# Optimization experiments

Hardware: AMD Instinct MI355X
Metric: run time of the kernel (lower is better)

The kernel has to match this reference:

```python
import jax, jax.numpy as jnp
import numpy as np

HIDDEN = 256
OUT_CH = 3
OMEGA_0 = 30.0
PATCH = 5


def setup_inputs() -> dict:
    key = jax.random.key(0)
    ks = jax.random.split(key, 9)
    B, C, H, W = 1, 128, 256, 256
    in_dim = C * PATCH * PATCH + 2  # 3202
    xi = jax.random.normal(ks[0], (B, C, H, W), dtype=jnp.float32)

    def lin(kw, kb, fi, fo):
        s = 1.0 / np.sqrt(fi)
        Wm = jax.random.uniform(kw, (fi, fo), jnp.float32, -s, s)
        bm = jax.random.uniform(kb, (fo,), jnp.float32, -s, s)
        return Wm, bm

    W1, b1 = lin(ks[1], ks[2], in_dim, HIDDEN)
    W2, b2 = lin(ks[3], ks[4], HIDDEN, HIDDEN)
    W3, b3 = lin(ks[5], ks[6], HIDDEN, HIDDEN)
    W4, b4 = lin(ks[7], ks[8], HIDDEN, OUT_CH)
    return {"xi": xi, "W1": W1, "b1": b1, "W2": W2, "b2": b2,
            "W3": W3, "b3": b3, "W4": W4, "b4": b4}


def _make_coords(B, H, W, dtype):
    # normalized pixel coords in [-1, 1], shape [B*H*W, 2]
    ys = jnp.linspace(-1.0, 1.0, H, dtype=dtype)
    xs = jnp.linspace(-1.0, 1.0, W, dtype=dtype)
    gy, gx = jnp.meshgrid(ys, xs, indexing="ij")
    coords = jnp.stack([gy, gx], axis=-1).reshape(H * W, 2)
    return jnp.tile(coords, (B, 1))


def reference(xi, W1, b1, W2, b2, W3, b3, W4, b4):
    B, C, H, W = xi.shape
    # im2col 5x5 patch gather (zero pad), like F.unfold with padding=2
    patches = jax.lax.conv_general_dilated_patches(
        xi, (PATCH, PATCH), (1, 1), "SAME")  # [B, C*25, H, W]
    feat = jnp.transpose(patches, (0, 2, 3, 1)).reshape(B * H * W, C * PATCH * PATCH)
    coords = _make_coords(B, H, W, xi.dtype)
    x = jnp.concatenate([feat, coords], axis=-1)  # [N, 3202]
    h = jnp.sin(OMEGA_0 * (x @ W1 + b1))
    h = jnp.sin(OMEGA_0 * (h @ W2 + b2))
    h = jnp.sin(OMEGA_0 * (h @ W3 + b3))
    out = h @ W4 + b4  # [N, 3]
    rgb = out.reshape(B, H, W, OUT_CH).transpose(0, 3, 1, 2)
    return rgb
```

## Files before the change

kernel.cpp:

```cpp
#include <hip/hip_runtime.h>
#include <math.h>
#include <stdint.h>

typedef _Float16 f16;
typedef _Float16 f16x8 __attribute__((ext_vector_type(8)));
typedef float f32x4 __attribute__((ext_vector_type(4)));
typedef unsigned short u16;
typedef u16 u16x8 __attribute__((ext_vector_type(8)));

#define HID 256
#define NS1C 100
#define NS2 8
#define NPX 65536
#define BPXG 256
#define NBG (NPX/BPXG)
#define SPAD 260
#define NSP (SPAD*SPAD)

#define OFF_W1C 0
#define SZ_W1C  ((size_t)NS1C*32768)
#define OFF_W2  SZ_W1C
#define SZ_W2   ((size_t)NS2*32768)
#define OFF_W3  (OFF_W2+SZ_W2)
#define OFF_XH  ((size_t)4194304)
#define SZ_XP   ((size_t)NSP*128*2)
#define OFF_XL  (OFF_XH + SZ_XP)
#define OFF_HH  (OFF_XL + SZ_XP)
#define SZ_HP   ((size_t)NPX*HID*2)
#define OFF_HL  (OFF_HH + SZ_HP)

__device__ inline void split2(float v, u16& h, u16& l){
  f16 hv = (f16)v;
  f16 lv = (f16)(v - (float)hv);
  h = __builtin_bit_cast(u16, hv);
  l = __builtin_bit_cast(u16, lv);
}

__global__ void prep_w(const float* __restrict__ W, int Kact, int nStages,
                       u16* __restrict__ outp){
  int t = blockIdx.x*256 + threadIdx.x;
  if (t >= nStages*1024) return;
  int s = t >> 10, r = t & 1023;
  int w = r >> 8, nf = (r >> 6) & 3, l = r & 63;
  int col = w*64 + nf*16 + (l & 15);
  int kb  = s*32 + (l >> 4)*8;
  u16x8 hv, lv;
  #pragma unroll
  for (int j = 0; j < 8; ++j){
    int k = kb + j;
    float v = (k < Kact) ? W[(size_t)k*HID + col] : 0.f;
    u16 h, lo; split2(v, h, lo);
    hv[j] = h; lv[j] = lo;
  }
  size_t U0 = ((((size_t)s*4 + w)*4 + nf)*2 + 0)*64 + l;
  *(u16x8*)(outp + U0*8)      = hv;
  *(u16x8*)(outp + (U0+64)*8) = lv;
}

__global__ void prep_w1c(const float* __restrict__ W1, u16* __restrict__ outp){
  int t = blockIdx.x*256 + threadIdx.x;
  if (t >= NS1C*1024) return;
  int s = t >> 10, r = t & 1023;
  int w = r >> 8, nf = (r >> 6) & 3, l = r & 63;
  int col = w*64 + nf*16 + (l & 15);
  int tap = s >> 2, cg = s & 3;
  int cb  = cg*32 + (l >> 4)*8;
  u16x8 hv, lv;
  #pragma unroll
  for (int j = 0; j < 8; ++j){
    int c = cb + j;
    float v = W1[(size_t)(c*25 + tap)*HID + col];
    u16 h, lo; split2(v, h, lo);
    hv[j] = h; lv[j] = lo;
  }
  size_t U0 = ((((size_t)s*4 + w)*4 + nf)*2 + 0)*64 + l;
  *(u16x8*)(outp + U0*8)      = hv;
  *(u16x8*)(outp + (U0+64)*8) = lv;
}

__global__ __launch_bounds__(256)
void prep_x(const float* __restrict__ xi, u16* __restrict__ Xh, u16* __restrict__ Xl){
  int sp = blockIdx.x*256 + threadIdx.x;
  if (sp >= NSP) return;
  int py = sp / SPAD;
  int px = sp - py*SPAD;
  bool inb = (py >= 2) & (py < 258) & (px >= 2) & (px < 258);
  const float* xin = xi + ((size_t)(py-2)<<8) + (px-2);
  #pragma unroll 4
  for (int cg = 0; cg < 16; ++cg){
    u16x8 hv, lv;
    #pragma unroll
    for (int j = 0; j < 8; ++j){
      float v = inb ? xin[((size_t)(cg*8 + j))<<16] : 0.f;
      u16 h, l; split2(v, h, l); hv[j] = h; lv[j] = l;
    }
    *(u16x8*)(Xh + (size_t)sp*128 + cg*8) = hv;
    *(u16x8*)(Xl + (size_t)sp*128 + cg*8) = lv;
  }
}

template<int MODE>
__global__ __launch_bounds__(512, 2)
void gemm(const u16* __restrict__ Ah, const u16* __restrict__ Al,
          const u16* __restrict__ Wp, const float* __restrict__ W1,
          const float* __restrict__ bias, u16* __restrict__ Hh, u16* __restrict__ Hl,
          const float* __restrict__ W4, const float* __restrict__ b4,
          float* __restrict__ out, int nt)
{
  __shared__ __align__(16) u16 Ab[2][16384];
  __shared__ __align__(16) u16 Bb[2][16384];

  const int tid  = threadIdx.x;
  const int lane = tid & 63;
  const int wv   = tid >> 6;
  const int wm   = wv >> 2, wn = wv & 3;

  int bid = blockIdx.x;
  bid = (bid & 7)*(NBG/8) + (bid >> 3);
  const int pxb = bid * BPXG;
  const int y   = bid;

  f32x4 acc[8][4];
  #pragma unroll
  for (int a=0;a<8;a++)
    #pragma unroll
    for (int bq=0;bq<4;bq++) acc[a][bq] = f32x4{0.f,0.f,0.f,0.f};

#define A_STAGE(S, BUF) do { \
    _Pragma("unroll") \
    for (int u=0;u<2;++u){ \
      const int mfb = wv*2 + u; \
      size_t off; \
      if (MODE == 0){ \
        const int tap = (S) >> 2, cg = (S) & 3; \
        const int dy = tap/5, dx = tap - 5*dy; \
        const int sp = (y + dy)*SPAD + dx + mfb*16 + (lane & 15); \
        off = (size_t)sp*128 + cg*32 + (lane >> 4)*8; \
      } else { \
        const int px = pxb + mfb*16 + (lane & 15); \
        off = (size_t)px*HID + (S)*32 + (lane >> 4)*8; \
      } \
      __builtin_amdgcn_global_load_lds( \
        (const __attribute__((address_space(1))) uint32_t*)(Ah + off), \
        (__attribute__((address_space(3))) uint32_t*)((char*)&Ab[BUF][0] + (mfb*2+0)*1024), \
        16, 0, 0); \
      __builtin_amdgcn_global_load_lds( \
        (const __attribute__((address_space(1))) uint32_t*)(Al + off), \
        (__attribute__((address_space(3))) uint32_t*)((char*)&Ab[BUF][0] + (mfb*2+1)*1024), \
        16, 0, 0); \
    } \
  } while(0)

#define B_STAGE(S, BUF) do { \
    const char* _src = (const char*)Wp + (size_t)(S)*32768 + wv*4096 + lane*16; \
    char* _dst = (char*)&Bb[BUF][0] + wv*4096; \
    _Pragma("unroll") \
    for (int i=0;i<4;++i) \
      __builtin_amdgcn_global_load_lds( \
        (const __attribute__((address_space(1))) uint32_t*)(_src + i*1024), \
        (__attribute__((address_space(3))) uint32_t*)(_dst + i*1024), 16, 0, 0); \
  } while(0)

  A_STAGE(0, 0); B_STAGE(0, 0);
  A_STAGE(1, 1); B_STAGE(1, 1);

  for (int t = 0; t < nt; ++t){
    if (t+1 < nt) { asm volatile("s_waitcnt vmcnt(8)" ::: "memory"); }
    else          { asm volatile("s_waitcnt vmcnt(0)" ::: "memory"); }
    __builtin_amdgcn_s_barrier();
    __builtin_amdgcn_sched_barrier(0);
    const int cur = t & 1;

    f16x8 bh[4], bl[4];
    #pragma unroll
    for (int nf=0;nf<4;++nf){
      bh[nf] = *(const f16x8*)(&Bb[cur][((size_t)((wn*4+nf)*2+0)*64 + lane)*8]);
      bl[nf] = *(const f16x8*)(&Bb[cur][((size_t)((wn*4+nf)*2+1)*64 + lane)*8]);
    }
    __builtin_amdgcn_s_setprio(1);
    #pragma unroll
    for (int mf=0;mf<8;++mf){
      const int mfb = wm*8 + mf;
      f16x8 ahf = *(const f16x8*)(&Ab[cur][((size_t)(mfb*2+0)*64 + lane)*8]);
      f16x8 alf = *(const f16x8*)(&Ab[cur][((size_t)(mfb*2+1)*64 + lane)*8]);
      #pragma unroll
      for (int nf=0;nf<4;++nf){
        acc[mf][nf] = __builtin_amdgcn_mfma_f32_16x16x32_f16(ahf, bh[nf], acc[mf][nf], 0,0,0);
        acc[mf][nf] = __builtin_amdgcn_mfma_f32_16x16x32_f16(alf, bh[nf], acc[mf][nf], 0,0,0);
        acc[mf][nf] = __builtin_amdgcn_mfma_f32_16x16x32_f16(ahf, bl[nf], acc[mf][nf], 0,0,0);
      }
    }
    __builtin_amdgcn_s_setprio(0);
    asm volatile("s_waitcnt lgkmcnt(0)" ::: "memory");
    __builtin_amdgcn_s_barrier();
    if (t+2 < nt){
      A_STAGE(t+2, cur);
      B_STAGE(t+2, cur);
    }
  }

  float bcol[4];
  #pragma unroll
  for (int nf=0;nf<4;++nf) bcol[nf] = bias[wn*64 + nf*16 + (lane&15)];

  if (MODE == 0){
    float wyv[4], wxv[4];
    #pragma unroll
    for (int nf=0;nf<4;++nf){
      int col = wn*64 + nf*16 + (lane&15);
      wyv[nf] = W1[(size_t)3200*HID + col];
      wxv[nf] = W1[(size_t)3201*HID + col];
    }
    const float gy = -1.f + (2.f/255.f)*(float)y;
    #pragma unroll
    for (int mf=0;mf<8;++mf)
      #pragma unroll
      for (int nf=0;nf<4;++nf)
        #pragma unroll
        for (int j=0;j<4;++j){
          int row = wm*128 + mf*16 + (lane>>4)*4 + j;
          float gx = -1.f + (2.f/255.f)*(float)row;
          float z = acc[mf][nf][j] + bcol[nf] + gy*wyv[nf] + gx*wxv[nf];
          float h = sinf(30.f*z);
          u16 hh,ll; split2(h,hh,ll);
          int col = wn*64 + nf*16 + (lane&15);
          size_t o = (size_t)(pxb+row)*HID + col;
          Hh[o] = hh; Hl[o] = ll;
        }
  } else if (MODE == 1){
    #pragma unroll
    for (int mf=0;mf<8;++mf)
      #pragma unroll
      for (int nf=0;nf<4;++nf)
        #pragma unroll
        for (int j=0;j<4;++j){
          float z = acc[mf][nf][j] + bcol[nf];
          float h = sinf(30.f*z);
          u16 hh,ll; split2(h,hh,ll);
          int row = wm*128 + mf*16 + (lane>>4)*4 + j;
          int col = wn*64 + nf*16 + (lane&15);
          size_t o = (size_t)(pxb+row)*HID + col;
          Hh[o] = hh; Hl[o] = ll;
        }
  } else {
    float (*red)[BPXG][3] = (float(*)[BPXG][3])(void*)&Ab[0][0];
    float w4v[4][3];
    #pragma unroll
    for (int nf=0;nf<4;++nf){
      int col = wn*64 + nf*16 + (lane&15);
      w4v[nf][0]=W4[col*3+0]; w4v[nf][1]=W4[col*3+1]; w4v[nf][2]=W4[col*3+2];
    }
    #pragma unroll
    for (int mf=0;mf<8;++mf)
      #pragma unroll
      for (int j=0;j<4;++j){
        float s0=0.f,s1=0.f,s2=0.f;
        #pragma unroll
        for (int nf=0;nf<4;++nf){
          float h = sinf(30.f*(acc[mf][nf][j] + bcol[nf]));
          s0 += h*w4v[nf][0]; s1 += h*w4v[nf][1]; s2 += h*w4v[nf][2];
        }
        #pragma unroll
        for (int m=1;m<16;m<<=1){
          s0 += __shfl_xor(s0, m);
          s1 += __shfl_xor(s1, m);
          s2 += __shfl_xor(s2, m);
        }
        if ((lane & 15) == 0){
          int row = wm*128 + mf*16 + (lane>>4)*4 + j;
          red[wn + wm*4][row][0]=s0; red[wn + wm*4][row][1]=s1; red[wn + wm*4][row][2]=s2;
        }
      }
    __syncthreads();
    for (int o = tid; o < BPXG*3; o += 512){
      int px = o & 255, c = o >> 8;
      int wb = (px >> 7)*4;
      float v = red[wb+0][px][c]+red[wb+1][px][c]+red[wb+2][px][c]+red[wb+3][px][c] + b4[c];
      out[(size_t)c*NPX + pxb + px] = v;
    }
  }
#undef A_STAGE
#undef B_STAGE
}

extern "C" void kernel_launch(void* const* d_in, const int* in_sizes, int n_in,
                              void* d_out, int out_size, void* d_ws, size_t ws_size,
                              hipStream_t stream) {
  const float* xi = (const float*)d_in[0];
  const float* W1 = (const float*)d_in[1];
  const float* b1 = (const float*)d_in[2];
  const float* W2 = (const float*)d_in[3];
  const float* b2 = (const float*)d_in[4];
  const float* W3 = (const float*)d_in[5];
  const float* b3 = (const float*)d_in[6];
  const float* W4 = (const float*)d_in[7];
  const float* b4 = (const float*)d_in[8];
  float* out = (float*)d_out;

  char* ws = (char*)d_ws;
  u16* W1c = (u16*)(ws + OFF_W1C);
  u16* W2p = (u16*)(ws + OFF_W2);
  u16* W3p = (u16*)(ws + OFF_W3);
  u16* Xh  = (u16*)(ws + OFF_XH);
  u16* Xl  = (u16*)(ws + OFF_XL);
  u16* Hh  = (u16*)(ws + OFF_HH);
  u16* Hl  = (u16*)(ws + OFF_HL);

  prep_w1c<<<NS1C*4, 256, 0, stream>>>(W1, W1c);
  prep_w<<<NS2*4, 256, 0, stream>>>(W2, HID, NS2, W2p);
  prep_w<<<NS2*4, 256, 0, stream>>>(W3, HID, NS2, W3p);
  prep_x<<<(NSP + 255)/256, 256, 0, stream>>>(xi, Xh, Xl);

  dim3 grid(NBG), block(512);
  gemm<0><<<grid, block, 0, stream>>>(Xh, Xl, W1c, W1, b1, Hh, Hl,
                                      nullptr, nullptr, nullptr, NS1C);
  gemm<1><<<grid, block, 0, stream>>>(Hh, Hl, W2p, nullptr, b2, Hh, Hl,
                                      nullptr, nullptr, nullptr, NS2);
  gemm<2><<<grid, block, 0, stream>>>(Hh, Hl, W3p, nullptr, b3, nullptr, nullptr,
                                      W4, b4, out, NS2);
}
```

Before: 488.8 us.

## Stage epilogue through LDS for coalesced hidden writes and simplify prefetch pipeline

```diff
diff --git a/kernel.cpp b/kernel.cpp
--- a/kernel.cpp
+++ b/kernel.cpp
@@ -107,8 +107,7 @@
           const float* __restrict__ W4, const float* __restrict__ b4,
           float* __restrict__ out, int nt)
 {
-  __shared__ __align__(16) u16 Ab[2][16384];
-  __shared__ __align__(16) u16 Bb[2][16384];
+  __shared__ __align__(16) u16 Sb[65536];
 
   const int tid  = threadIdx.x;
   const int lane = tid & 63;
@@ -142,18 +141,18 @@
       } \
       __builtin_amdgcn_global_load_lds( \
         (const __attribute__((address_space(1))) uint32_t*)(Ah + off), \
-        (__attribute__((address_space(3))) uint32_t*)((char*)&Ab[BUF][0] + (mfb*2+0)*1024), \
+        (__attribute__((address_space(3))) uint32_t*)((char*)Sb + (size_t)(BUF)*32768 + (mfb*2+0)*1024), \
         16, 0, 0); \
       __builtin_amdgcn_global_load_lds( \
         (const __attribute__((address_space(1))) uint32_t*)(Al + off), \
-        (__attribute__((address_space(3))) uint32_t*)((char*)&Ab[BUF][0] + (mfb*2+1)*1024), \
+        (__attribute__((address_space(3))) uint32_t*)((char*)Sb + (size_t)(BUF)*32768 + (mfb*2+1)*1024), \
         16, 0, 0); \
     } \
   } while(0)
 
 #define B_STAGE(S, BUF) do { \
     const char* _src = (const char*)Wp + (size_t)(S)*32768 + wv*4096 + lane*16; \
-    char* _dst = (char*)&Bb[BUF][0] + wv*4096; \
+    char* _dst = (char*)Sb + 65536 + (size_t)(BUF)*32768 + wv*4096; \
     _Pragma("unroll") \
     for (int i=0;i<4;++i) \
       __builtin_amdgcn_global_load_lds( \
@@ -162,27 +161,32 @@
   } while(0)
 
   A_STAGE(0, 0); B_STAGE(0, 0);
-  A_STAGE(1, 1); B_STAGE(1, 1);
 
   for (int t = 0; t < nt; ++t){
-    if (t+1 < nt) { asm volatile("s_waitcnt vmcnt(8)" ::: "memory"); }
-    else          { asm volatile("s_waitcnt vmcnt(0)" ::: "memory"); }
+    asm volatile("s_waitcnt vmcnt(0)" ::: "memory");
     __builtin_amdgcn_s_barrier();
     __builtin_amdgcn_sched_barrier(0);
     const int cur = t & 1;
+    if (t+1 < nt){
+      A_STAGE(t+1, cur^1);
+      B_STAGE(t+1, cur^1);
+    }
+
+    const u16* Abuf = (const u16*)Sb + (size_t)cur*16384;
+    const u16* Bbuf = (const u16*)Sb + 32768 + (size_t)cur*16384;
 
     f16x8 bh[4], bl[4];
     #pragma unroll
     for (int nf=0;nf<4;++nf){
-      bh[nf] = *(const f16x8*)(&Bb[cur][((size_t)((wn*4+nf)*2+0)*64 + lane)*8]);
-      bl[nf] = *(const f16x8*)(&Bb[cur][((size_t)((wn*4+nf)*2+1)*64 + lane)*8]);
+      bh[nf] = *(const f16x8*)(Bbuf + ((size_t)((wn*4+nf)*2+0)*64 + lane)*8);
+      bl[nf] = *(const f16x8*)(Bbuf + ((size_t)((wn*4+nf)*2+1)*64 + lane)*8);
     }
     __builtin_amdgcn_s_setprio(1);
     #pragma unroll
     for (int mf=0;mf<8;++mf){
       const int mfb = wm*8 + mf;
-      f16x8 ahf = *(const f16x8*)(&Ab[cur][((size_t)(mfb*2+0)*64 + lane)*8]);
-      f16x8 alf = *(const f16x8*)(&Ab[cur][((size_t)(mfb*2+1)*64 + lane)*8]);
+      f16x8 ahf = *(const f16x8*)(Abuf + ((size_t)(mfb*2+0)*64 + lane)*8);
+      f16x8 alf = *(const f16x8*)(Abuf + ((size_t)(mfb*2+1)*64 + lane)*8);
       #pragma unroll
       for (int nf=0;nf<4;++nf){
         acc[mf][nf] = __builtin_amdgcn_mfma_f32_16x16x32_f16(ahf, bh[nf], acc[mf][nf], 0,0,0);
@@ -191,59 +195,74 @@
       }
     }
     __builtin_amdgcn_s_setprio(0);
-    asm volatile("s_waitcnt lgkmcnt(0)" ::: "memory");
-    __builtin_amdgcn_s_barrier();
-    if (t+2 < nt){
-      A_STAGE(t+2, cur);
-      B_STAGE(t+2, cur);
-    }
-  }
+  }
+
+  __syncthreads();
 
   float bcol[4];
   #pragma unroll
   for (int nf=0;nf<4;++nf) bcol[nf] = bias[wn*64 + nf*16 + (lane&15)];
 
-  if (MODE == 0){
-    float wyv[4], wxv[4];
-    #pragma unroll
-    for (int nf=0;nf<4;++nf){
-      int col = wn*64 + nf*16 + (lane&15);
-      wyv[nf] = W1[(size_t)3200*HID + col];
-      wxv[nf] = W1[(size_t)3201*HID + col];
-    }
-    const float gy = -1.f + (2.f/255.f)*(float)y;
-    #pragma unroll
-    for (int mf=0;mf<8;++mf)
+  if (MODE == 0 || MODE == 1){
+    float wyv[4], wxv[4], gy = 0.f;
+    if (MODE == 0){
       #pragma unroll
-      for (int nf=0;nf<4;++nf)
+      for (int nf=0;nf<4;++nf){
+        int col = wn*64 + nf*16 + (lane&15);
+        wyv[nf] = W1[(size_t)3200*HID + col];
+        wxv[nf] = W1[(size_t)3201*HID + col];
+      }
+      gy = -1.f + (2.f/255.f)*(float)y;
+    }
+    uint32_t* Tr = (uint32_t*)Sb;
+    #pragma unroll
+    for (int hf=0; hf<2; ++hf){
+      if (wm == hf){
         #pragma unroll
-        for (int j=0;j<4;++j){
-          int row = wm*128 + mf*16 + (lane>>4)*4 + j;
-          float gx = -1.f + (2.f/255.f)*(float)row;
-          float z = acc[mf][nf][j] + bcol[nf] + gy*wyv[nf] + gx*wxv[nf];
-          float h = sinf(30.f*z);
-          u16 hh,ll; split2(h,hh,ll);
-          int col = wn*64 + nf*16 + (lane&15);
-          size_t o = (size_t)(pxb+row)*HID + col;
-          Hh[o] = hh; Hl[o] = ll;
-        }
-  } else if (MODE == 1){
-    #pragma unroll
-    for (int mf=0;mf<8;++mf)
+        for (int mf=0;mf<8;++mf)
+          #pragma unroll
+          for (int nf=0;nf<4;++nf)
+            #pragma unroll
+            for (int j=0;j<4;++j){
+              int rl  = mf*16 + (lane>>4)*4 + j;
+              int col = wn*64 + nf*16 + (lane&15);
+              float z = acc[mf][nf][j] + bcol[nf];
+              if (MODE == 0){
+                int row = hf*128 + rl;
+                float gx = -1.f + (2.f/255.f)*(float)row;
+                z += gy*wyv[nf] + gx*wxv[nf];
+              }
+              float h = sinf(30.f*z);
+              u16 hh, ll; split2(h, hh, ll);
+              Tr[rl*256 + col] = (uint32_t)hh | ((uint32_t)ll << 16);
+            }
+      }
+      __syncthreads();
       #pragma unroll
-      for (int nf=0;nf<4;++nf)
-        #pragma unroll
-        for (int j=0;j<4;++j){
-          float z = acc[mf][nf][j] + bcol[nf];
-          float h = sinf(30.f*z);
-          u16 hh,ll; split2(h,hh,ll);
-          int row = wm*128 + mf*16 + (lane>>4)*4 + j;
-          int col = wn*64 + nf*16 + (lane&15);
-          size_t o = (size_t)(pxb+row)*HID + col;
-          Hh[o] = hh; Hl[o] = ll;
-        }
+      for (int i=0;i<8;++i){
+        int u  = i*512 + tid;
+        int r  = u >> 5;
+        int cu = (u & 31) * 8;
+        const uint32_t* p = Tr + r*256 + cu;
+        uint4 a0 = *(const uint4*)p;
+        uint4 a1 = *(const uint4*)(p+4);
+        u16x8 vh, vl;
+        vh[0]=(u16)a0.x; vl[0]=(u16)(a0.x>>16);
+        vh[1]=(u16)a0.y; vl[1]=(u16)(a0.y>>16);
+        vh[2]=(u16)a0.z; vl[2]=(u16)(a0.z>>16);
+        vh[3]=(u16)a0.w; vl[3]=(u16)(a0.w>>16);
+        vh[4]=(u16)a1.x; vl[4]=(u16)(a1.x>>16);
+        vh[5]=(u16)a1.y; vl[5]=(u16)(a1.y>>16);
+        vh[6]=(u16)a1.z; vl[6]=(u16)(a1.z>>16);
+        vh[7]=(u16)a1.w; vl[7]=(u16)(a1.w>>16);
+        size_t px = (size_t)(pxb + hf*128 + r);
+        *(u16x8*)(Hh + px*HID + cu) = vh;
+        *(u16x8*)(Hl + px*HID + cu) = vl;
+      }
+      __syncthreads();
+    }
   } else {
-    float (*red)[BPXG][3] = (float(*)[BPXG][3])(void*)&Ab[0][0];
+    float (*red)[BPXG][3] = (float(*)[BPXG][3])(void*)Sb;
     float w4v[4][3];
     #pragma unroll
     for (int nf=0;nf<4;++nf){
```

Measured after the change: 506.9 us. +3.7%, slower.

## Restructure GEMM double-buffer to a single barrier per k-step with grouped MFMA issue

Applied to the files above, without the earlier changes.

```diff
diff --git a/kernel.cpp b/kernel.cpp
--- a/kernel.cpp
+++ b/kernel.cpp
@@ -107,8 +107,7 @@
           const float* __restrict__ W4, const float* __restrict__ b4,
           float* __restrict__ out, int nt)
 {
-  __shared__ __align__(16) u16 Ab[2][16384];
-  __shared__ __align__(16) u16 Bb[2][16384];
+  __shared__ __align__(16) u16 Sb[65536];
 
   const int tid  = threadIdx.x;
   const int lane = tid & 63;
@@ -142,18 +141,18 @@
       } \
       __builtin_amdgcn_global_load_lds( \
         (const __attribute__((address_space(1))) uint32_t*)(Ah + off), \
-        (__attribute__((address_space(3))) uint32_t*)((char*)&Ab[BUF][0] + (mfb*2+0)*1024), \
+        (__attribute__((address_space(3))) uint32_t*)((char*)Sb + (size_t)(BUF)*32768 + (mfb*2+0)*1024), \
         16, 0, 0); \
       __builtin_amdgcn_global_load_lds( \
         (const __attribute__((address_space(1))) uint32_t*)(Al + off), \
-        (__attribute__((address_space(3))) uint32_t*)((char*)&Ab[BUF][0] + (mfb*2+1)*1024), \
+        (__attribute__((address_space(3))) uint32_t*)((char*)Sb + (size_t)(BUF)*32768 + (mfb*2+1)*1024), \
         16, 0, 0); \
     } \
   } while(0)
 
 #define B_STAGE(S, BUF) do { \
     const char* _src = (const char*)Wp + (size_t)(S)*32768 + wv*4096 + lane*16; \
-    char* _dst = (char*)&Bb[BUF][0] + wv*4096; \
+    char* _dst = (char*)Sb + 65536 + (size_t)(BUF)*32768 + wv*4096; \
     _Pragma("unroll") \
     for (int i=0;i<4;++i) \
       __builtin_amdgcn_global_load_lds( \
@@ -162,42 +161,56 @@
   } while(0)
 
   A_STAGE(0, 0); B_STAGE(0, 0);
-  A_STAGE(1, 1); B_STAGE(1, 1);
 
   for (int t = 0; t < nt; ++t){
-    if (t+1 < nt) { asm volatile("s_waitcnt vmcnt(8)" ::: "memory"); }
-    else          { asm volatile("s_waitcnt vmcnt(0)" ::: "memory"); }
+    asm volatile("s_waitcnt vmcnt(0)" ::: "memory");
     __builtin_amdgcn_s_barrier();
     __builtin_amdgcn_sched_barrier(0);
     const int cur = t & 1;
+    if (t+1 < nt){
+      A_STAGE(t+1, cur^1);
+      B_STAGE(t+1, cur^1);
+    }
+
+    const u16* Abuf = (const u16*)Sb + (size_t)cur*16384;
+    const u16* Bbuf = (const u16*)Sb + 32768 + (size_t)cur*16384;
 
     f16x8 bh[4], bl[4];
     #pragma unroll
     for (int nf=0;nf<4;++nf){
-      bh[nf] = *(const f16x8*)(&Bb[cur][((size_t)((wn*4+nf)*2+0)*64 + lane)*8]);
-      bl[nf] = *(const f16x8*)(&Bb[cur][((size_t)((wn*4+nf)*2+1)*64 + lane)*8]);
+      bh[nf] = *(const f16x8*)(Bbuf + ((size_t)((wn*4+nf)*2+0)*64 + lane)*8);
+      bl[nf] = *(const f16x8*)(Bbuf + ((size_t)((wn*4+nf)*2+1)*64 + lane)*8);
     }
     __builtin_amdgcn_s_setprio(1);
     #pragma unroll
-    for (int mf=0;mf<8;++mf){
-      const int mfb = wm*8 + mf;
-      f16x8 ahf = *(const f16x8*)(&Ab[cur][((size_t)(mfb*2+0)*64 + lane)*8]);
-      f16x8 alf = *(const f16x8*)(&Ab[cur][((size_t)(mfb*2+1)*64 + lane)*8]);
-      #pragma unroll
-      for (int nf=0;nf<4;++nf){
-        acc[mf][nf] = __builtin_amdgcn_mfma_f32_16x16x32_f16(ahf, bh[nf], acc[mf][nf], 0,0,0);
-        acc[mf][nf] = __builtin_amdgcn_mfma_f32_16x16x32_f16(alf, bh[nf], acc[mf][nf], 0,0,0);
-        acc[mf][nf] = __builtin_amdgcn_mfma_f32_16x16x32_f16(ahf, bl[nf], acc[mf][nf], 0,0,0);
+    for (int hf=0; hf<2; ++hf){
+      f16x8 ahv[4], alv[4];
+      #pragma unroll
+      for (int m=0;m<4;++m){
+        const int mfb = wm*8 + hf*4 + m;
+        ahv[m] = *(const f16x8*)(Abuf + ((size_t)(mfb*2+0)*64 + lane)*8);
+        alv[m] = *(const f16x8*)(Abuf + ((size_t)(mfb*2+1)*64 + lane)*8);
       }
+      #pragma unroll
+      for (int m=0;m<4;++m)
+        #pragma unroll
+        for (int nf=0;nf<4;++nf)
+          acc[hf*4+m][nf] = __builtin_amdgcn_mfma_f32_16x16x32_f16(ahv[m], bh[nf], acc[hf*4+m][nf], 0,0,0);
+      #pragma unroll
+      for (int m=0;m<4;++m)
+        #pragma unroll
+        for (int nf=0;nf<4;++nf)
+          acc[hf*4+m][nf] = __builtin_amdgcn_mfma_f32_16x16x32_f16(alv[m], bh[nf], acc[hf*4+m][nf], 0,0,0);
+      #pragma unroll
+      for (int m=0;m<4;++m)
+        #pragma unroll
+        for (int nf=0;nf<4;++nf)
+          acc[hf*4+m][nf] = __builtin_amdgcn_mfma_f32_16x16x32_f16(ahv[m], bl[nf], acc[hf*4+m][nf], 0,0,0);
     }
     __builtin_amdgcn_s_setprio(0);
-    asm volatile("s_waitcnt lgkmcnt(0)" ::: "memory");
-    __builtin_amdgcn_s_barrier();
-    if (t+2 < nt){
-      A_STAGE(t+2, cur);
-      B_STAGE(t+2, cur);
-    }
-  }
+  }
+
+  __syncthreads();
 
   float bcol[4];
   #pragma unroll
@@ -243,7 +256,7 @@
           Hh[o] = hh; Hl[o] = ll;
         }
   } else {
-    float (*red)[BPXG][3] = (float(*)[BPXG][3])(void*)&Ab[0][0];
+    float (*red)[BPXG][3] = (float(*)[BPXG][3])(void*)Sb;
     float w4v[4][3];
     #pragma unroll
     for (int nf=0;nf<4;++nf){
```

Result: faster. 471.1 us (-3.6%).
